# Kernel tuning notes

Measured on AMD Instinct MI355X. Metric: run time of the kernel, lower is better.

## Reference

```python
import jax, jax.numpy as jnp
import numpy as np


def setup_inputs() -> dict:
    key = jax.random.key(0)
    ks = jax.random.split(key, 8)
    B, T, IN, H, OUT = 64, 512, 256, 1024, 256
    s_in = 1.0 / np.sqrt(IN)
    s_h = 1.0 / np.sqrt(H)
    return {
        "X": jax.random.normal(ks[0], (B, T, IN), jnp.float32),
        "Wx": jax.random.normal(ks[1], (H, IN), jnp.float32) * s_in,
        "bx": jnp.zeros((H,), jnp.float32),
        "Wh": jax.random.normal(ks[2], (H, H), jnp.float32) * s_h,
        "Uz": jax.random.normal(ks[3], (H, IN), jnp.float32) * s_in,
        "bz": jnp.zeros((H,), jnp.float32),
        "Vz": jax.random.normal(ks[4], (H, H), jnp.float32) * s_h,
        "Ur": jax.random.normal(ks[5], (H, IN), jnp.float32) * s_in,
        "br": jnp.zeros((H,), jnp.float32),
        "Vr": jax.random.normal(ks[6], (H, H), jnp.float32) * s_h,
        "Wo": jax.random.normal(ks[7], (OUT, H), jnp.float32) * s_h,
        "bo": jnp.zeros((OUT,), jnp.float32),
    }


def reference(X, Wx, bx, Wh, Uz, bz, Vz, Ur, br, Vr, Wo, bo):
    # Nonstandard GRU from philip-bl/tensor_train_rnn: gates (z, r) are
    # computed AFTER the hidden-state update, so gate values from timestep
    # t-1 modulate the update at timestep t. h, r, z all start at zero.
    B, T, _ = X.shape
    H = Wx.shape[0]
    # Batch all input projections into three big GEMMs up-front: [B,T,H]
    x_h = jnp.einsum("bti,hi->bth", X, Wx) + bx
    x_z = jnp.einsum("bti,hi->bth", X, Uz) + bz
    x_r = jnp.einsum("bti,hi->bth", X, Ur) + br

    def step(carry, inp):
        h, r, z = carry
        xh, xz, xr = inp  # each [B,H]
        h_tilde = jnp.tanh(xh + (h * r) @ Wh.T)  # tanh activation, dropout p=0 is identity
        h = z * h + (1.0 - z) * h_tilde
        z = jax.nn.sigmoid(xz + h @ Vz.T)
        r = jax.nn.sigmoid(xr + h @ Vr.T)
        return (h, r, z), None

    zeros = jnp.zeros((B, H), X.dtype)
    xs = (jnp.swapaxes(x_h, 0, 1), jnp.swapaxes(x_z, 0, 1), jnp.swapaxes(x_r, 0, 1))  # [T,B,H]
    (h, _, _), _ = jax.lax.scan(step, (zeros, zeros, zeros), xs)
    return h @ Wo.T + bo  # [B, OUT]
```

## Files before the change

kernel.cpp:

```cpp
#include <hip/hip_runtime.h>


#define BB 64
#define TT 512
#define KIN 256
#define HH 1024
#define NOUT 256

typedef float  f32x4 __attribute__((ext_vector_type(4)));
typedef short  s16x8 __attribute__((ext_vector_type(8)));
typedef unsigned int u32x4 __attribute__((ext_vector_type(4)));
typedef unsigned short u16x4 __attribute__((ext_vector_type(4)));

#define MFMA16(a, b, c) __builtin_amdgcn_mfma_f32_16x16x32_bf16((a), (b), (c), 0, 0, 0)

static __device__ __forceinline__ s16x8 as16(u32x4 v) { return __builtin_bit_cast(s16x8, v); }

static __device__ __forceinline__ unsigned short f2bf(float f) {
  unsigned u = __float_as_uint(f);
  u += 0x7FFFu + ((u >> 16) & 1u);
  return (unsigned short)(u >> 16);
}
static __device__ __forceinline__ float bf2f(unsigned short h) {
  return __uint_as_float(((unsigned)h) << 16);
}

static __device__ __forceinline__ float tanh_fast(float x) {
  float xc = fminf(fmaxf(x, -15.f), 15.f);
  float e = __expf(2.f * xc);
  return (e - 1.f) / (e + 1.f);
}
static __device__ __forceinline__ float sigmoid_fast(float x) {
  float xc = fminf(fmaxf(x, -30.f), 30.f);
  return 1.f / (1.f + __expf(-xc));
}

static __device__ __forceinline__ void st_dw(unsigned* p, unsigned v) {
  asm volatile("global_store_dword %0, %1, off sc0 sc1" :: "v"(p), "v"(v) : "memory");
}
template <int OFF>
static __device__ __forceinline__ void ld128o(u32x4& d, const unsigned* p) {
  asm volatile("global_load_dwordx4 %0, %1, off offset:%2 sc0 sc1"
               : "=v"(d) : "v"(p), "i"(OFF));
}
static __device__ __forceinline__ void tie16(u32x4& a0, u32x4& a1, u32x4& a2, u32x4& a3,
                                             u32x4& a4, u32x4& a5, u32x4& a6, u32x4& a7,
                                             u32x4& a8, u32x4& a9, u32x4& aA, u32x4& aB,
                                             u32x4& aC, u32x4& aD, u32x4& aE, u32x4& aF) {
  asm volatile("s_waitcnt vmcnt(0)"
               : "+v"(a0), "+v"(a1), "+v"(a2), "+v"(a3),
                 "+v"(a4), "+v"(a5), "+v"(a6), "+v"(a7),
                 "+v"(a8), "+v"(a9), "+v"(aA), "+v"(aB),
                 "+v"(aC), "+v"(aD), "+v"(aE), "+v"(aF)
               :: "memory");
}

static __device__ __forceinline__ unsigned pk(unsigned hi, unsigned lo) {
  return __builtin_amdgcn_perm(hi, lo, 0x07060302u);
}
static __device__ __forceinline__ u32x4 pack_frag(u32x4 a, u32x4 b) {
  u32x4 r;
  r.x = pk(a.y, a.x); r.y = pk(a.w, a.z);
  r.z = pk(b.y, b.x); r.w = pk(b.w, b.z);
  return r;
}

static __device__ __forceinline__ void load_validated(
    const unsigned* rp0, unsigned tag, bool& dead, u32x4 (&a)[8]) {
  const unsigned* p1 = rp0 + 1024;
  const unsigned* p2 = rp0 + 2048;
  const unsigned* p3 = rp0 + 3072;
  u32x4 r0, r1, r2, r3, r4, r5, r6, r7, r8, r9, rA, rB, rC, rD, rE, rF;
  int guard = 0;
  while (true) {
    ld128o<0>(r0, rp0); ld128o<1024>(r1, rp0); ld128o<2048>(r2, rp0); ld128o<3072>(r3, rp0);
    ld128o<0>(r4, p1);  ld128o<1024>(r5, p1);  ld128o<2048>(r6, p1);  ld128o<3072>(r7, p1);
    ld128o<0>(r8, p2);  ld128o<1024>(r9, p2);  ld128o<2048>(rA, p2);  ld128o<3072>(rB, p2);
    ld128o<0>(rC, p3);  ld128o<1024>(rD, p3);  ld128o<2048>(rE, p3);  ld128o<3072>(rF, p3);
    tie16(r0, r1, r2, r3, r4, r5, r6, r7, r8, r9, rA, rB, rC, rD, rE, rF);
    unsigned bad = 0;
#define CHK(R) bad |= (R.x ^ tag) | (R.y ^ tag) | (R.z ^ tag) | (R.w ^ tag)
    CHK(r0); CHK(r1); CHK(r2); CHK(r3); CHK(r4); CHK(r5); CHK(r6); CHK(r7);
    CHK(r8); CHK(r9); CHK(rA); CHK(rB); CHK(rC); CHK(rD); CHK(rE); CHK(rF);
#undef CHK
    bad &= 0xFFFFu;
    if (__all(bad == 0)) break;
    if (dead || ++guard > 4096) { dead = true; break; }
  }
  a[0] = pack_frag(r0, r1); a[1] = pack_frag(r2, r3);
  a[2] = pack_frag(r4, r5); a[3] = pack_frag(r6, r7);
  a[4] = pack_frag(r8, r9); a[5] = pack_frag(rA, rB);
  a[6] = pack_frag(rC, rD); a[7] = pack_frag(rE, rF);
}

static constexpr size_t SZ_XP   = (size_t)TT * BB * HH * 2;
static constexpr size_t OFF_XH  = 0;
static constexpr size_t OFF_XZ  = OFF_XH + SZ_XP;
static constexpr size_t OFF_XR  = OFF_XZ + SZ_XP;
static constexpr size_t OFF_XB  = OFF_XR + SZ_XP;
static constexpr size_t OFF_WHP = OFF_XB + (size_t)BB * TT * KIN * 2;
static constexpr size_t OFF_VZP = OFF_WHP + (size_t)HH * HH * 2;
static constexpr size_t OFF_VRP = OFF_VZP + (size_t)HH * HH * 2;
static constexpr size_t OFF_WXP = OFF_VRP + (size_t)HH * HH * 2;
static constexpr size_t OFF_UZP = OFF_WXP + (size_t)HH * KIN * 2;
static constexpr size_t OFF_URP = OFF_UZP + (size_t)HH * KIN * 2;
static constexpr size_t OFF_HB  = OFF_URP + (size_t)HH * KIN * 2;
static constexpr size_t OFF_HRB = OFF_HB + (size_t)4 * 16 * HH * 4;
static constexpr size_t OFF_HF  = OFF_HRB + (size_t)4 * 16 * HH * 4;

__global__ void __launch_bounds__(256) k_convert_x(const float* __restrict__ X,
                                                   unsigned short* __restrict__ Xb) {
  size_t i = ((size_t)blockIdx.x * 256 + threadIdx.x) * 4;
  f32x4 v = *(const f32x4*)(X + i);
  u16x4 o = { f2bf(v[0]), f2bf(v[1]), f2bf(v[2]), f2bf(v[3]) };
  *(u16x4*)(Xb + i) = o;
}

__global__ void __launch_bounds__(256) k_pack_w(
    const float* __restrict__ Wh, const float* __restrict__ Vz, const float* __restrict__ Vr,
    const float* __restrict__ Wx, const float* __restrict__ Uz, const float* __restrict__ Ur,
    unsigned short* __restrict__ Whp, unsigned short* __restrict__ Vzp, unsigned short* __restrict__ Vrp,
    unsigned short* __restrict__ Wxp, unsigned short* __restrict__ Uzp, unsigned short* __restrict__ Urp) {
  int z = blockIdx.y;
  const float* src; unsigned short* dst; int K;
  switch (z) {
    case 0: src = Wh; dst = Whp; K = 1024; break;
    case 1: src = Vz; dst = Vzp; K = 1024; break;
    case 2: src = Vr; dst = Vrp; K = 1024; break;
    case 3: src = Wx; dst = Wxp; K = 256;  break;
    case 4: src = Uz; dst = Uzp; K = 256;  break;
    default: src = Ur; dst = Urp; K = 256; break;
  }
  int KK = K >> 5;
  int total = 64 * KK * 64;
  int tau = blockIdx.x * 256 + threadIdx.x;
  if (tau >= total) return;
  int lane = tau & 63;
  int kk = (tau >> 6) % KK;
  int ct = tau / (KK * 64);
  int q = lane >> 4, cl = lane & 15;
  const float* s = src + (size_t)(ct * 16 + cl) * K + kk * 32 + q * 8;
  f32x4 v0 = *(const f32x4*)s;
  f32x4 v1 = *(const f32x4*)(s + 4);
  u32x4 o;
  o.x = (unsigned)f2bf(v0[0]) | ((unsigned)f2bf(v0[1]) << 16);
  o.y = (unsigned)f2bf(v0[2]) | ((unsigned)f2bf(v0[3]) << 16);
  o.z = (unsigned)f2bf(v1[0]) | ((unsigned)f2bf(v1[1]) << 16);
  o.w = (unsigned)f2bf(v1[2]) | ((unsigned)f2bf(v1[3]) << 16);
  *(u32x4*)(dst + (size_t)tau * 8) = o;
}

__global__ void __launch_bounds__(256) k_proj(
    const unsigned short* __restrict__ Xb,
    const unsigned short* __restrict__ Wxp, const unsigned short* __restrict__ Uzp,
    const unsigned short* __restrict__ Urp,
    const float* __restrict__ bx, const float* __restrict__ bz, const float* __restrict__ br,
    unsigned short* __restrict__ XH, unsigned short* __restrict__ XZ, unsigned short* __restrict__ XR) {
  __shared__ u32x4 As[4 * 8 * 64];
  const int tid = threadIdx.x;
  const int mb = blockIdx.x, cb = blockIdx.y, mu = blockIdx.z;

#pragma unroll
  for (int i = 0; i < 8; ++i) {
    int fid = i * 256 + tid;
    int lane = fid & 63, kk = (fid >> 6) & 7, rt = fid >> 9;
    int q = lane >> 4, cl = lane & 15;
    int mrow = mb * 64 + rt * 16 + cl;
    As[fid] = *(const u32x4*)(Xb + (size_t)mrow * KIN + kk * 32 + q * 8);
  }
  __syncthreads();

  const int lane = tid & 63, w = tid >> 6;
  const int q = lane >> 4, cl = lane & 15;
  const unsigned short* Bp = (mu == 0) ? Wxp : (mu == 1) ? Uzp : Urp;
  const float* bias        = (mu == 0) ? bx  : (mu == 1) ? bz  : br;
  unsigned short* Dst      = (mu == 0) ? XH  : (mu == 1) ? XZ  : XR;

  f32x4 z4 = {0.f, 0.f, 0.f, 0.f};
  f32x4 acc[4] = {z4, z4, z4, z4};
  const int ctg = cb * 4 + w;
#pragma unroll
  for (int kk = 0; kk < 8; ++kk) {
    u32x4 b = *(const u32x4*)(Bp + ((size_t)(ctg * 8 + kk) * 64 + lane) * 8);
#pragma unroll
    for (int rt = 0; rt < 4; ++rt)
      acc[rt] = MFMA16(as16(As[(rt * 8 + kk) * 64 + lane]), as16(b), acc[rt]);
  }
  const int col = cb * 64 + w * 16 + cl;
  const float bv = bias[col];
#pragma unroll
  for (int rt = 0; rt < 4; ++rt) {
#pragma unroll
    for (int j = 0; j < 4; ++j) {
      int m = mb * 64 + rt * 16 + q * 4 + j;
      int t = m & (TT - 1), b = m >> 9;
      Dst[((size_t)t * BB + b) * HH + col] = f2bf(acc[rt][j] + bv);
    }
  }
}

__global__ void __launch_bounds__(256, 1) k_scan(
    const unsigned short* __restrict__ XH, const unsigned short* __restrict__ XZ,
    const unsigned short* __restrict__ XR,
    const unsigned short* __restrict__ Whp, const unsigned short* __restrict__ Vzp,
    const unsigned short* __restrict__ Vrp,
    unsigned* __restrict__ hb32all, unsigned* __restrict__ hrb32all,
    float* __restrict__ hfinal) {
  __shared__ f32x4 redA[16 * 64];
  __shared__ f32x4 redB[16 * 64];
  __shared__ f32x4 redC[16 * 64];

  const int tid = threadIdx.x;
  const int lane = tid & 63, w = tid >> 6;
  const int q = lane >> 4, cl = lane & 15;
  const int blk = blockIdx.x;
  const int g = blk >> 4, c = blk & 15;
  const int c4 = c * 4, kw = w * 8;

  unsigned* hb  = hb32all  + (size_t)g * 16 * HH;
  unsigned* hrb = hrb32all + (size_t)g * 16 * HH;

  u32x4 wh[4][8], vz[4][8];
#pragma unroll
  for (int ct = 0; ct < 4; ++ct)
#pragma unroll
    for (int k = 0; k < 8; ++k) {
      size_t fi = (((size_t)(c4 + ct) * 32 + kw + k) * 64 + lane) * 8;
      wh[ct][k] = *(const u32x4*)(Whp + fi);
      vz[ct][k] = *(const u32x4*)(Vzp + fi);
    }

  const int hcol = c * 64 + w * 16 + cl;
  const int brow0 = g * 16 + q * 4;

  const unsigned* rpA = hrb + w * 4096 + lane * 4;
  const unsigned* rpB = hb  + w * 4096 + lane * 4;
  const unsigned C = (unsigned)hcol;
  const unsigned sbase = ((C >> 8) * 8 + ((C >> 5) & 7)) * 512 + ((C >> 2) & 1) * 256 +
                         (((C >> 3) & 3) * 16 + q * 4) * 4 + (C & 3);
  unsigned* spA = hb  + sbase;
  unsigned* spB = hrb + sbase;

  const f32x4 z4 = {0.f, 0.f, 0.f, 0.f};
  f32x4 hreg = z4, zreg = z4;
  bool dead = false;

  for (int t = 0; t < TT; ++t) {
    unsigned short xh_u[4];
#pragma unroll
    for (int j = 0; j < 4; ++j)
      xh_u[j] = XH[((size_t)t * BB + brow0 + j) * HH + hcol];

    f32x4 acc[4] = {z4, z4, z4, z4};
    if (t > 0) {
      u32x4 a[8];
      load_validated(rpA, (unsigned)t, dead, a);
#pragma unroll
      for (int k = 0; k < 8; ++k) {
        s16x8 av = as16(a[k]);
#pragma unroll
        for (int ct = 0; ct < 4; ++ct)
          acc[ct] = MFMA16(av, as16(wh[ct][k]), acc[ct]);
      }
    }
#pragma unroll
    for (int ct = 0; ct < 4; ++ct) redA[(w * 4 + ct) * 64 + lane] = acc[ct];
    __syncthreads();
    f32x4 S = redA[(0 * 4 + w) * 64 + lane];
    S += redA[(1 * 4 + w) * 64 + lane];
    S += redA[(2 * 4 + w) * 64 + lane];
    S += redA[(3 * 4 + w) * 64 + lane];

    const unsigned tagn = (unsigned)(t + 1);
    if (t == TT - 1) {
#pragma unroll
      for (int j = 0; j < 4; ++j) {
        float pre = S[j] + bf2f(xh_u[j]);
        float ht = tanh_fast(pre);
        hreg[j] = zreg[j] * hreg[j] + (1.f - zreg[j]) * ht;
      }
      break;
    }
#pragma unroll
    for (int j = 0; j < 4; ++j) {
      float pre = S[j] + bf2f(xh_u[j]);
      float ht = tanh_fast(pre);
      float hn = zreg[j] * hreg[j] + (1.f - zreg[j]) * ht;
      hreg[j] = hn;
      st_dw(spA + j * 4, ((unsigned)f2bf(hn) << 16) | tagn);
    }

    unsigned short xz_u[4], xr_u[4];
#pragma unroll
    for (int j = 0; j < 4; ++j) {
      xz_u[j] = XZ[((size_t)t * BB + brow0 + j) * HH + hcol];
      xr_u[j] = XR[((size_t)t * BB + brow0 + j) * HH + hcol];
    }
    u32x4 b[8];
    load_validated(rpB, tagn, dead, b);

    f32x4 az[4] = {z4, z4, z4, z4};
    f32x4 ar[4] = {z4, z4, z4, z4};
#pragma unroll
    for (int ct = 0; ct < 4; ++ct) {
      u32x4 vrk[8];
#pragma unroll
      for (int k = 0; k < 8; ++k)
        vrk[k] = *(const u32x4*)(Vrp + (((size_t)(c4 + ct) * 32 + kw + k) * 64 + lane) * 8);
#pragma unroll
      for (int k = 0; k < 8; ++k)
        az[ct] = MFMA16(as16(b[k]), as16(vz[ct][k]), az[ct]);
#pragma unroll
      for (int k = 0; k < 8; ++k)
        ar[ct] = MFMA16(as16(b[k]), as16(vrk[k]), ar[ct]);
    }
#pragma unroll
    for (int ct = 0; ct < 4; ++ct) {
      redB[(w * 4 + ct) * 64 + lane] = az[ct];
      redC[(w * 4 + ct) * 64 + lane] = ar[ct];
    }
    __syncthreads();
    f32x4 Sz = redB[(0 * 4 + w) * 64 + lane];
    Sz += redB[(1 * 4 + w) * 64 + lane];
    Sz += redB[(2 * 4 + w) * 64 + lane];
    Sz += redB[(3 * 4 + w) * 64 + lane];
    f32x4 Sr = redC[(0 * 4 + w) * 64 + lane];
    Sr += redC[(1 * 4 + w) * 64 + lane];
    Sr += redC[(2 * 4 + w) * 64 + lane];
    Sr += redC[(3 * 4 + w) * 64 + lane];

#pragma unroll
    for (int j = 0; j < 4; ++j) {
      float zv = sigmoid_fast(Sz[j] + bf2f(xz_u[j]));
      float rv = sigmoid_fast(Sr[j] + bf2f(xr_u[j]));
      zreg[j] = zv;
      st_dw(spB + j * 4, ((unsigned)f2bf(rv * hreg[j]) << 16) | tagn);
    }
  }

#pragma unroll
  for (int j = 0; j < 4; ++j)
    hfinal[(size_t)(brow0 + j) * HH + hcol] = hreg[j];
}

__global__ void __launch_bounds__(256) k_out(const float* __restrict__ hf,
                                             const float* __restrict__ Wo,
                                             const float* __restrict__ bo,
                                             float* __restrict__ out) {
  __shared__ float hs[HH];
  const int b = blockIdx.x, tid = threadIdx.x;
  *(f32x4*)&hs[tid * 4] = *(const f32x4*)(hf + (size_t)b * HH + tid * 4);
  __syncthreads();
  float acc = bo[tid];
  const f32x4* wr = (const f32x4*)(Wo + (size_t)tid * HH);
#pragma unroll 8
  for (int k = 0; k < HH / 4; ++k) {
    f32x4 wv = wr[k];
    f32x4 hv = *(const f32x4*)&hs[k * 4];
    acc += wv[0] * hv[0] + wv[1] * hv[1] + wv[2] * hv[2] + wv[3] * hv[3];
  }
  out[(size_t)b * NOUT + tid] = acc;
}

extern "C" void kernel_launch(void* const* d_in, const int* in_sizes, int n_in,
                              void* d_out, int out_size, void* d_ws, size_t ws_size,
                              hipStream_t stream) {
  (void)in_sizes; (void)n_in; (void)out_size; (void)ws_size;
  const float* X  = (const float*)d_in[0];
  const float* Wx = (const float*)d_in[1];
  const float* bx = (const float*)d_in[2];
  const float* Wh = (const float*)d_in[3];
  const float* Uz = (const float*)d_in[4];
  const float* bz = (const float*)d_in[5];
  const float* Vz = (const float*)d_in[6];
  const float* Ur = (const float*)d_in[7];
  const float* br = (const float*)d_in[8];
  const float* Vr = (const float*)d_in[9];
  const float* Wo = (const float*)d_in[10];
  const float* bo = (const float*)d_in[11];

  char* ws = (char*)d_ws;
  unsigned short* XHp = (unsigned short*)(ws + OFF_XH);
  unsigned short* XZp = (unsigned short*)(ws + OFF_XZ);
  unsigned short* XRp = (unsigned short*)(ws + OFF_XR);
  unsigned short* Xb  = (unsigned short*)(ws + OFF_XB);
  unsigned short* Whp = (unsigned short*)(ws + OFF_WHP);
  unsigned short* Vzp = (unsigned short*)(ws + OFF_VZP);
  unsigned short* Vrp = (unsigned short*)(ws + OFF_VRP);
  unsigned short* Wxp = (unsigned short*)(ws + OFF_WXP);
  unsigned short* Uzp = (unsigned short*)(ws + OFF_UZP);
  unsigned short* Urp = (unsigned short*)(ws + OFF_URP);
  unsigned* hbp  = (unsigned*)(ws + OFF_HB);
  unsigned* hrbp = (unsigned*)(ws + OFF_HRB);
  float* hfp = (float*)(ws + OFF_HF);

  k_convert_x<<<8192, 256, 0, stream>>>(X, Xb);
  k_pack_w<<<dim3(512, 6), 256, 0, stream>>>(Wh, Vz, Vr, Wx, Uz, Ur,
                                             Whp, Vzp, Vrp, Wxp, Uzp, Urp);
  k_proj<<<dim3(512, 16, 3), 256, 0, stream>>>(Xb, Wxp, Uzp, Urp, bx, bz, br,
                                               XHp, XZp, XRp);
  k_scan<<<64, 256, 0, stream>>>(XHp, XZp, XRp, Whp, Vzp, Vrp,
                                 hbp, hrbp, hfp);
  k_out<<<64, 256, 0, stream>>>(hfp, Wo, bo, (float*)d_out);
}
```

Measured before the change: 4.015 ms.

## Place each scan group on one XCD and use XCD-local coherence for exchange

The scan kernel now launches 128 blocks and maps block index so each 16-block batch group is likely to land on a single XCD (round-robin dispatch). It checks this at runtime by reading HW_REG_XCC_ID, then runs a two-phase handshake. If all 16 blocks agree, the per-step hidden-state exchange uses sc0-only loads and stores (L2-scoped) instead of sc0 sc1 system-coherent ones, which should cut the latency of the cross-block flag polling. It adds a ctrl init kernel and startup synchronization, and depends on the dispatch-placement assumption holding.

```diff
diff --git a/kernel.cpp b/kernel.cpp
--- a/kernel.cpp
+++ b/kernel.cpp
@@ -35,14 +35,41 @@
   return 1.f / (1.f + __expf(-xc));
 }
 
+template <bool LOCAL>
 static __device__ __forceinline__ void st_dw(unsigned* p, unsigned v) {
+  if (LOCAL)
+    asm volatile("global_store_dword %0, %1, off sc0" :: "v"(p), "v"(v) : "memory");
+  else
+    asm volatile("global_store_dword %0, %1, off sc0 sc1" :: "v"(p), "v"(v) : "memory");
+}
+template <bool LOCAL, int OFF>
+static __device__ __forceinline__ void ld128o(u32x4& d, const unsigned* p) {
+  if (LOCAL)
+    asm volatile("global_load_dwordx4 %0, %1, off offset:%2 sc0"
+                 : "=v"(d) : "v"(p), "i"(OFF));
+  else
+    asm volatile("global_load_dwordx4 %0, %1, off offset:%2 sc0 sc1"
+                 : "=v"(d) : "v"(p), "i"(OFF));
+}
+static __device__ __forceinline__ void st_dw_sys(unsigned* p, unsigned v) {
   asm volatile("global_store_dword %0, %1, off sc0 sc1" :: "v"(p), "v"(v) : "memory");
 }
-template <int OFF>
-static __device__ __forceinline__ void ld128o(u32x4& d, const unsigned* p) {
-  asm volatile("global_load_dwordx4 %0, %1, off offset:%2 sc0 sc1"
-               : "=v"(d) : "v"(p), "i"(OFF));
-}
+static __device__ __forceinline__ unsigned ld_dw_sys(const unsigned* p) {
+  unsigned v;
+  asm volatile("global_load_dword %0, %1, off sc0 sc1\n\ts_waitcnt vmcnt(0)"
+               : "=v"(v) : "v"(p) : "memory");
+  return v;
+}
+static __device__ __forceinline__ void st_dw_sc0(unsigned* p, unsigned v) {
+  asm volatile("global_store_dword %0, %1, off sc0" :: "v"(p), "v"(v) : "memory");
+}
+static __device__ __forceinline__ unsigned ld_dw_sc0(const unsigned* p) {
+  unsigned v;
+  asm volatile("global_load_dword %0, %1, off sc0\n\ts_waitcnt vmcnt(0)"
+               : "=v"(v) : "v"(p) : "memory");
+  return v;
+}
+
 static __device__ __forceinline__ void tie16(u32x4& a0, u32x4& a1, u32x4& a2, u32x4& a3,
                                              u32x4& a4, u32x4& a5, u32x4& a6, u32x4& a7,
                                              u32x4& a8, u32x4& a9, u32x4& aA, u32x4& aB,
@@ -65,6 +92,7 @@
   return r;
 }
 
+template <bool LOCAL>
 static __device__ __forceinline__ void load_validated(
     const unsigned* rp0, unsigned tag, bool& dead, u32x4 (&a)[8]) {
   const unsigned* p1 = rp0 + 1024;
@@ -73,10 +101,14 @@
   u32x4 r0, r1, r2, r3, r4, r5, r6, r7, r8, r9, rA, rB, rC, rD, rE, rF;
   int guard = 0;
   while (true) {
-    ld128o<0>(r0, rp0); ld128o<1024>(r1, rp0); ld128o<2048>(r2, rp0); ld128o<3072>(r3, rp0);
-    ld128o<0>(r4, p1);  ld128o<1024>(r5, p1);  ld128o<2048>(r6, p1);  ld128o<3072>(r7, p1);
-    ld128o<0>(r8, p2);  ld128o<1024>(r9, p2);  ld128o<2048>(rA, p2);  ld128o<3072>(rB, p2);
-    ld128o<0>(rC, p3);  ld128o<1024>(rD, p3);  ld128o<2048>(rE, p3);  ld128o<3072>(rF, p3);
+    ld128o<LOCAL,0>(r0, rp0); ld128o<LOCAL,1024>(r1, rp0);
+    ld128o<LOCAL,2048>(r2, rp0); ld128o<LOCAL,3072>(r3, rp0);
+    ld128o<LOCAL,0>(r4, p1);  ld128o<LOCAL,1024>(r5, p1);
+    ld128o<LOCAL,2048>(r6, p1);  ld128o<LOCAL,3072>(r7, p1);
+    ld128o<LOCAL,0>(r8, p2);  ld128o<LOCAL,1024>(r9, p2);
+    ld128o<LOCAL,2048>(rA, p2);  ld128o<LOCAL,3072>(rB, p2);
+    ld128o<LOCAL,0>(rC, p3);  ld128o<LOCAL,1024>(rD, p3);
+    ld128o<LOCAL,2048>(rE, p3);  ld128o<LOCAL,3072>(rF, p3);
     tie16(r0, r1, r2, r3, r4, r5, r6, r7, r8, r9, rA, rB, rC, rD, rE, rF);
     unsigned bad = 0;
 #define CHK(R) bad |= (R.x ^ tag) | (R.y ^ tag) | (R.z ^ tag) | (R.w ^ tag)
@@ -85,7 +117,7 @@
 #undef CHK
     bad &= 0xFFFFu;
     if (__all(bad == 0)) break;
-    if (dead || ++guard > 4096) { dead = true; break; }
+    if (dead || ++guard > 8192) { dead = true; break; }
   }
   a[0] = pack_frag(r0, r1); a[1] = pack_frag(r2, r3);
   a[2] = pack_frag(r4, r5); a[3] = pack_frag(r6, r7);
@@ -107,6 +139,9 @@
 static constexpr size_t OFF_HB  = OFF_URP + (size_t)HH * KIN * 2;
 static constexpr size_t OFF_HRB = OFF_HB + (size_t)4 * 16 * HH * 4;
 static constexpr size_t OFF_HF  = OFF_HRB + (size_t)4 * 16 * HH * 4;
+static constexpr size_t OFF_CTRL = OFF_HF + (size_t)BB * HH * 4;
+
+__global__ void k_init(unsigned* __restrict__ ctrl) { ctrl[threadIdx.x] = 0u; }
 
 __global__ void __launch_bounds__(256) k_convert_x(const float* __restrict__ X,
                                                    unsigned short* __restrict__ Xb) {
@@ -199,22 +234,18 @@
   }
 }
 
-__global__ void __launch_bounds__(256, 1) k_scan(
+template <bool LOCAL>
+static __device__ __forceinline__ void scan_loop(
+    const int tid, const int g, const int c,
     const unsigned short* __restrict__ XH, const unsigned short* __restrict__ XZ,
     const unsigned short* __restrict__ XR,
     const unsigned short* __restrict__ Whp, const unsigned short* __restrict__ Vzp,
     const unsigned short* __restrict__ Vrp,
     unsigned* __restrict__ hb32all, unsigned* __restrict__ hrb32all,
-    float* __restrict__ hfinal) {
-  __shared__ f32x4 redA[16 * 64];
-  __shared__ f32x4 redB[16 * 64];
-  __shared__ f32x4 redC[16 * 64];
-
-  const int tid = threadIdx.x;
+    float* __restrict__ hfinal,
+    f32x4* redA, f32x4* redB, f32x4* redC) {
   const int lane = tid & 63, w = tid >> 6;
   const int q = lane >> 4, cl = lane & 15;
-  const int blk = blockIdx.x;
-  const int g = blk >> 4, c = blk & 15;
   const int c4 = c * 4, kw = w * 8;
 
   unsigned* hb  = hb32all  + (size_t)g * 16 * HH;
@@ -254,7 +285,7 @@
     f32x4 acc[4] = {z4, z4, z4, z4};
     if (t > 0) {
       u32x4 a[8];
-      load_validated(rpA, (unsigned)t, dead, a);
+      load_validated<LOCAL>(rpA, (unsigned)t, dead, a);
 #pragma unroll
       for (int k = 0; k < 8; ++k) {
         s16x8 av = as16(a[k]);
@@ -287,7 +318,7 @@
       float ht = tanh_fast(pre);
       float hn = zreg[j] * hreg[j] + (1.f - zreg[j]) * ht;
       hreg[j] = hn;
-      st_dw(spA + j * 4, ((unsigned)f2bf(hn) << 16) | tagn);
+      st_dw<LOCAL>(spA + j * 4, ((unsigned)f2bf(hn) << 16) | tagn);
     }
 
     unsigned short xz_u[4], xr_u[4];
@@ -297,7 +328,7 @@
       xr_u[j] = XR[((size_t)t * BB + brow0 + j) * HH + hcol];
     }
     u32x4 b[8];
-    load_validated(rpB, tagn, dead, b);
+    load_validated<LOCAL>(rpB, tagn, dead, b);
 
     f32x4 az[4] = {z4, z4, z4, z4};
     f32x4 ar[4] = {z4, z4, z4, z4};
@@ -334,13 +365,95 @@
       float zv = sigmoid_fast(Sz[j] + bf2f(xz_u[j]));
       float rv = sigmoid_fast(Sr[j] + bf2f(xr_u[j]));
       zreg[j] = zv;
-      st_dw(spB + j * 4, ((unsigned)f2bf(rv * hreg[j]) << 16) | tagn);
+      st_dw<LOCAL>(spB + j * 4, ((unsigned)f2bf(rv * hreg[j]) << 16) | tagn);
     }
   }
 
 #pragma unroll
   for (int j = 0; j < 4; ++j)
     hfinal[(size_t)(brow0 + j) * HH + hcol] = hreg[j];
+}
+
+__global__ void __launch_bounds__(256, 1) k_scan(
+    const unsigned short* __restrict__ XH, const unsigned short* __restrict__ XZ,
+    const unsigned short* __restrict__ XR,
+    const unsigned short* __restrict__ Whp, const unsigned short* __restrict__ Vzp,
+    const unsigned short* __restrict__ Vrp,
+    unsigned* __restrict__ hb32all, unsigned* __restrict__ hrb32all,
+    float* __restrict__ hfinal, unsigned* __restrict__ ctrl) {
+  __shared__ f32x4 redA[16 * 64];
+  __shared__ f32x4 redB[16 * 64];
+  __shared__ f32x4 redC[16 * 64];
+  __shared__ int shp[4];
+
+  const int blk = blockIdx.x;
+  const int g = blk & 7, c = blk >> 3;
+  if (g >= 4) return;
+  const int tid = threadIdx.x;
+
+  if (tid == 0) {
+    unsigned* xcb = ctrl;
+    unsigned* prb = ctrl + 64;
+    unsigned* okc = ctrl + 128;
+    unsigned* dnc = ctrl + 132;
+
+    unsigned xcc;
+    asm volatile("s_getreg_b32 %0, hwreg(HW_REG_XCC_ID)" : "=s"(xcc));
+    xcc &= 15u;
+    st_dw_sys(&xcb[g * 16 + c], 0x100u | xcc);
+    unsigned vals[16];
+    bool got = true;
+    for (int i = 0; i < 16; ++i) {
+      unsigned v = 0; int gd = 0;
+      do {
+        v = ld_dw_sys(&xcb[g * 16 + i]);
+        if (++gd > (1 << 20)) { got = false; break; }
+        if (!(v & 0x100u)) __builtin_amdgcn_s_sleep(2);
+      } while (!(v & 0x100u));
+      vals[i] = v & 0xFFu;
+      if (!got) break;
+    }
+    bool same = got;
+    if (got)
+      for (int i = 1; i < 16; ++i) same = same && (vals[i] == vals[0]);
+
+    unsigned s = 0;
+    if (same) {
+      st_dw_sc0(&prb[g * 16 + c], 1u);
+      bool ok1 = true;
+      for (int i = 0; i < 16 && ok1; ++i) {
+        int gd = 0;
+        while (ld_dw_sc0(&prb[g * 16 + i]) < 1u) {
+          if (++gd > (1 << 14)) { ok1 = false; break; }
+        }
+      }
+      if (ok1) {
+        st_dw_sc0(&prb[g * 16 + c], 2u);
+        bool ok2 = true;
+        for (int i = 0; i < 16 && ok2; ++i) {
+          int gd = 0;
+          while (ld_dw_sc0(&prb[g * 16 + i]) < 2u) {
+            if (++gd > (1 << 14)) { ok2 = false; break; }
+          }
+        }
+        s = ok2 ? 1u : 0u;
+      }
+    }
+    atomicAdd(&okc[g], s);
+    atomicAdd(&dnc[g], 1u);
+    while (atomicAdd(&dnc[g], 0u) < 16u) __builtin_amdgcn_s_sleep(4);
+    unsigned okv = atomicAdd(&okc[g], 0u);
+    shp[0] = (okv == 16u) ? 1 : 0;
+  }
+  __syncthreads();
+  const int loc = shp[0];
+
+  if (loc)
+    scan_loop<true>(tid, g, c, XH, XZ, XR, Whp, Vzp, Vrp,
+                    hb32all, hrb32all, hfinal, redA, redB, redC);
+  else
+    scan_loop<false>(tid, g, c, XH, XZ, XR, Whp, Vzp, Vrp,
+                     hb32all, hrb32all, hfinal, redA, redB, redC);
 }
 
 __global__ void __launch_bounds__(256) k_out(const float* __restrict__ hf,
@@ -393,13 +506,15 @@
   unsigned* hbp  = (unsigned*)(ws + OFF_HB);
   unsigned* hrbp = (unsigned*)(ws + OFF_HRB);
   float* hfp = (float*)(ws + OFF_HF);
-
+  unsigned* ctrl = (unsigned*)(ws + OFF_CTRL);
+
+  k_init<<<1, 256, 0, stream>>>(ctrl);
   k_convert_x<<<8192, 256, 0, stream>>>(X, Xb);
   k_pack_w<<<dim3(512, 6), 256, 0, stream>>>(Wh, Vz, Vr, Wx, Uz, Ur,
                                              Whp, Vzp, Vrp, Wxp, Uzp, Urp);
   k_proj<<<dim3(512, 16, 3), 256, 0, stream>>>(Xb, Wxp, Uzp, Urp, bx, bz, br,
                                                XHp, XZp, XRp);
-  k_scan<<<64, 256, 0, stream>>>(XHp, XZp, XRp, Whp, Vzp, Vrp,
-                                 hbp, hrbp, hfp);
+  k_scan<<<128, 256, 0, stream>>>(XHp, XZp, XRp, Whp, Vzp, Vrp,
+                                  hbp, hrbp, hfp, ctrl);
   k_out<<<64, 256, 0, stream>>>(hfp, Wo, bo, (float*)d_out);
 }
```

New measurement: 6.109 ms. 52.2% more time.

## Defer z-gate GEMM off critical path, publish r*h earlier

Applied to the files above, without the earlier changes.

Reorders each recurrent step so that only the r-gate GEMM runs before r*h is stored for the other blocks. The z-gate GEMM and its reduction are moved after that store and finished at the start of the next step, where z is first needed. The first Vr tile load is also hoisted ahead of the validated-load spin. The aim is to shorten the cross-block dependency chain per timestep, so dependent workgroups can start the next Wh GEMM sooner. The cost is that redB is now reused across iterations, which relies on the next step's barrier to order those accesses.

```diff
diff --git a/kernel.cpp b/kernel.cpp
--- a/kernel.cpp
+++ b/kernel.cpp
@@ -243,6 +243,7 @@
 
   const f32x4 z4 = {0.f, 0.f, 0.f, 0.f};
   f32x4 hreg = z4, zreg = z4;
+  unsigned short xz_u[4] = {0, 0, 0, 0};
   bool dead = false;
 
   for (int t = 0; t < TT; ++t) {
@@ -271,71 +272,85 @@
     S += redA[(2 * 4 + w) * 64 + lane];
     S += redA[(3 * 4 + w) * 64 + lane];
 
-    const unsigned tagn = (unsigned)(t + 1);
-    if (t == TT - 1) {
-#pragma unroll
-      for (int j = 0; j < 4; ++j) {
-        float pre = S[j] + bf2f(xh_u[j]);
-        float ht = tanh_fast(pre);
-        hreg[j] = zreg[j] * hreg[j] + (1.f - zreg[j]) * ht;
-      }
-      break;
-    }
+    if (t > 0) {
+      f32x4 Sz = redB[(0 * 4 + w) * 64 + lane];
+      Sz += redB[(1 * 4 + w) * 64 + lane];
+      Sz += redB[(2 * 4 + w) * 64 + lane];
+      Sz += redB[(3 * 4 + w) * 64 + lane];
+#pragma unroll
+      for (int j = 0; j < 4; ++j)
+        zreg[j] = sigmoid_fast(Sz[j] + bf2f(xz_u[j]));
+    }
+
+    float hn[4];
 #pragma unroll
     for (int j = 0; j < 4; ++j) {
       float pre = S[j] + bf2f(xh_u[j]);
       float ht = tanh_fast(pre);
-      float hn = zreg[j] * hreg[j] + (1.f - zreg[j]) * ht;
-      hreg[j] = hn;
-      st_dw(spA + j * 4, ((unsigned)f2bf(hn) << 16) | tagn);
-    }
-
-    unsigned short xz_u[4], xr_u[4];
+      hn[j] = zreg[j] * hreg[j] + (1.f - zreg[j]) * ht;
+      hreg[j] = hn[j];
+    }
+    if (t == TT - 1) break;
+
+    const unsigned tagn = (unsigned)(t + 1);
+#pragma unroll
+    for (int j = 0; j < 4; ++j)
+      st_dw(spA + j * 4, ((unsigned)f2bf(hn[j]) << 16) | tagn);
+
+    unsigned short xr_u[4];
 #pragma unroll
     for (int j = 0; j < 4; ++j) {
       xz_u[j] = XZ[((size_t)t * BB + brow0 + j) * HH + hcol];
       xr_u[j] = XR[((size_t)t * BB + brow0 + j) * HH + hcol];
     }
+    u32x4 vr0[8];
+#pragma unroll
+    for (int k = 0; k < 8; ++k)
+      vr0[k] = *(const u32x4*)(Vrp + (((size_t)(c4 + 0) * 32 + kw + k) * 64 + lane) * 8);
+
     u32x4 b[8];
     load_validated(rpB, tagn, dead, b);
 
-    f32x4 az[4] = {z4, z4, z4, z4};
     f32x4 ar[4] = {z4, z4, z4, z4};
 #pragma unroll
-    for (int ct = 0; ct < 4; ++ct) {
+    for (int k = 0; k < 8; ++k)
+      ar[0] = MFMA16(as16(b[k]), as16(vr0[k]), ar[0]);
+#pragma unroll
+    for (int ct = 1; ct < 4; ++ct) {
       u32x4 vrk[8];
 #pragma unroll
       for (int k = 0; k < 8; ++k)
         vrk[k] = *(const u32x4*)(Vrp + (((size_t)(c4 + ct) * 32 + kw + k) * 64 + lane) * 8);
 #pragma unroll
       for (int k = 0; k < 8; ++k)
-        az[ct] = MFMA16(as16(b[k]), as16(vz[ct][k]), az[ct]);
-#pragma unroll
-      for (int k = 0; k < 8; ++k)
         ar[ct] = MFMA16(as16(b[k]), as16(vrk[k]), ar[ct]);
     }
 #pragma unroll
-    for (int ct = 0; ct < 4; ++ct) {
-      redB[(w * 4 + ct) * 64 + lane] = az[ct];
-      redC[(w * 4 + ct) * 64 + lane] = ar[ct];
-    }
+    for (int ct = 0; ct < 4; ++ct) redC[(w * 4 + ct) * 64 + lane] = ar[ct];
     __syncthreads();
-    f32x4 Sz = redB[(0 * 4 + w) * 64 + lane];
-    Sz += redB[(1 * 4 + w) * 64 + lane];
-    Sz += redB[(2 * 4 + w) * 64 + lane];
-    Sz += redB[(3 * 4 + w) * 64 + lane];
     f32x4 Sr = redC[(0 * 4 + w) * 64 + lane];
     Sr += redC[(1 * 4 + w) * 64 + lane];
     Sr += redC[(2 * 4 + w) * 64 + lane];
     Sr += redC[(3 * 4 + w) * 64 + lane];
 
+    float rh[4];
 #pragma unroll
     for (int j = 0; j < 4; ++j) {
-      float zv = sigmoid_fast(Sz[j] + bf2f(xz_u[j]));
       float rv = sigmoid_fast(Sr[j] + bf2f(xr_u[j]));
-      zreg[j] = zv;
-      st_dw(spB + j * 4, ((unsigned)f2bf(rv * hreg[j]) << 16) | tagn);
-    }
+      rh[j] = rv * hreg[j];
+    }
+#pragma unroll
+    for (int j = 0; j < 4; ++j)
+      st_dw(spB + j * 4, ((unsigned)f2bf(rh[j]) << 16) | tagn);
+
+    f32x4 az[4] = {z4, z4, z4, z4};
+#pragma unroll
+    for (int ct = 0; ct < 4; ++ct)
+#pragma unroll
+      for (int k = 0; k < 8; ++k)
+        az[ct] = MFMA16(as16(b[k]), as16(vz[ct][k]), az[ct]);
+#pragma unroll
+    for (int ct = 0; ct < 4; ++ct) redB[(w * 4 + ct) * 64 + lane] = az[ct];
   }
 
 #pragma unroll
```

New measurement: 3.797 ms. -5.4%, faster.
